# Optimization experiments

Hardware: AMD Instinct MI355X
Metric: run time of the kernel (lower is better)

## Reference

```python
import jax, jax.numpy as jnp
import numpy as np

B, S, D = 2, 2048, 1024
H = 16
HD = D // H  # head_dim = 64


def setup_inputs() -> dict:
    key = jax.random.key(0)
    ks = jax.random.split(key, 6)
    scale = 0.02
    x = jax.random.normal(ks[0], (B, S, D), dtype=jnp.float32)
    Wq = jax.random.normal(ks[1], (D, D), dtype=jnp.float32) * scale
    Wk = jax.random.normal(ks[2], (D, D), dtype=jnp.float32) * scale
    Wv = jax.random.normal(ks[3], (D, D), dtype=jnp.float32) * scale
    Wo = jax.random.normal(ks[4], (D, D), dtype=jnp.float32) * scale
    bo = jax.random.normal(ks[5], (D,), dtype=jnp.float32) * scale
    return {"x": x, "Wq": Wq, "Wk": Wk, "Wv": Wv, "Wo": Wo, "bo": bo}


def reference(x, Wq, Wk, Wv, Wo, bo):
    b, s, d = x.shape
    # QKV projections (no bias, qkv_bias=False)
    Q = (x @ Wq).reshape(b, s, H, HD)
    K = (x @ Wk).reshape(b, s, H, HD)
    V = (x @ Wv).reshape(b, s, H, HD)
    # [b, h, q, k] attention scores
    scores = jnp.einsum('bqhd,bkhd->bhqk', Q, K)
    # causal mask: positions k > q masked to -inf (applied before scaling, as in source;
    # -inf / sqrt(hd) is still -inf so this matches)
    causal = jnp.triu(jnp.ones((s, s), dtype=bool), k=1)
    scores = jnp.where(causal, -jnp.inf, scores)
    att = jax.nn.softmax(scores / jnp.sqrt(jnp.float32(HD)), axis=-1)
    # dropout p=0.0 -> identity
    ctx = jnp.einsum('bhqk,bkhd->bqhd', att, V).reshape(b, s, d)
    return ctx @ Wo + bo
```

## Files before the change

kernel.cpp:

```cpp
#include <hip/hip_runtime.h>

typedef __bf16 bf16;
typedef __attribute__((ext_vector_type(8))) __bf16 bf16x8;
typedef __attribute__((ext_vector_type(4))) __bf16 bf16x4;
typedef __attribute__((ext_vector_type(4))) float floatx4;

#define MFMA16(a, b, c) __builtin_amdgcn_mfma_f32_16x16x32_bf16((a), (b), (c), 0, 0, 0)

static constexpr int BB = 2, SS = 2048, DD = 1024, HH = 16;
static constexpr int MM = BB * SS;
static constexpr int N_QKV = 3 * DD;

__device__ __forceinline__ float exp2c(float x) {
#if __has_builtin(__builtin_amdgcn_exp2f)
    return __builtin_amdgcn_exp2f(x);
#else
    return exp2f(x);
#endif
}

__device__ __forceinline__ void async16(const void* g, void* l) {
    __builtin_amdgcn_global_load_lds(
        (const __attribute__((address_space(1))) unsigned int*)g,
        (__attribute__((address_space(3))) unsigned int*)l, 16, 0, 0);
}

__global__ __launch_bounds__(256) void cvt_x_kernel(const float* __restrict__ x,
                                                    bf16* __restrict__ xb) {
    int i = (blockIdx.x * 256 + threadIdx.x) * 4;
    float4 v = *(const float4*)(x + i);
    bf16x4 o;
    o[0] = (bf16)v.x; o[1] = (bf16)v.y; o[2] = (bf16)v.z; o[3] = (bf16)v.w;
    *(bf16x4*)(xb + i) = o;
}

__global__ __launch_bounds__(256) void cvt_wT_kernel(const float* __restrict__ w0,
                                                     const float* __restrict__ w1,
                                                     const float* __restrict__ w2,
                                                     const float* __restrict__ w3,
                                                     bf16* __restrict__ outT) {
    __shared__ float tile[32][33];
    const float* src = (blockIdx.z == 0) ? w0 : (blockIdx.z == 1) ? w1
                      : (blockIdx.z == 2) ? w2 : w3;
    bf16* dst = outT + (size_t)blockIdx.z * DD * DD;
    int x = blockIdx.x * 32 + threadIdx.x;
    int y0 = blockIdx.y * 32;
    for (int i = threadIdx.y; i < 32; i += 8)
        tile[i][threadIdx.x] = src[(size_t)(y0 + i) * DD + x];
    __syncthreads();
    int xo = y0 + threadIdx.x;
    int yo0 = blockIdx.x * 32;
    for (int i = threadIdx.y; i < 32; i += 8)
        dst[(size_t)(yo0 + i) * DD + xo] = (bf16)tile[threadIdx.x][i];
}

__global__ __launch_bounds__(256) void transpose_v_kernel(const bf16* __restrict__ QKV,
                                                          bf16* __restrict__ Vt_g) {
    __shared__ bf16 t[64][72];
    const int tid = threadIdx.x, srow = tid >> 2, sseg = tid & 3;
    const int bh = blockIdx.y, b = bh >> 4, h = bh & 15;
    const int s0 = blockIdx.x * 64;
    {
        const uint4* p = (const uint4*)(QKV + (size_t)(b * SS + s0 + srow) * N_QKV
                                        + 2 * DD + h * 64 + sseg * 16);
        uint4 a = p[0], c = p[1];
        uint4* d = (uint4*)&t[srow][sseg * 16];
        d[0] = a; d[1] = c;
    }
    __syncthreads();
    bf16x8 o0, o1;
#pragma unroll
    for (int e = 0; e < 8; ++e) o0[e] = t[sseg * 16 + e][srow];
#pragma unroll
    for (int e = 0; e < 8; ++e) o1[e] = t[sseg * 16 + 8 + e][srow];
    uint4* d = (uint4*)(Vt_g + ((size_t)bh * 64 + srow) * SS + s0 + sseg * 16);
    d[0] = *(uint4*)&o0; d[1] = *(uint4*)&o1;
}

template <int BM, int BN, bool OUT_BF16>
__global__ __launch_bounds__(256) void gemm_kernel(const bf16* __restrict__ A,
                                                   const bf16* __restrict__ Bt,
                                                   void* __restrict__ C,
                                                   const float* __restrict__ bias,
                                                   int K, int ldc) {
    constexpr int MT = BM / 32, NT = BN / 32;
    __shared__ bf16 As[BM * 64];
    __shared__ bf16 Bs[BN * 64];
    const int tid = threadIdx.x, wave = tid >> 6, lane = tid & 63;
    const int quad = lane >> 4, l16 = lane & 15;
    const int wm = wave >> 1, wn = wave & 1;
    const int m0 = blockIdx.y * BM, n0 = blockIdx.x * BN;
    const int l8r = lane >> 3, l8c = lane & 7;
    const int gch = ((l8c ^ l8r) * 8);

    floatx4 acc[MT][NT] = {};

    for (int k0 = 0; k0 < K; k0 += 64) {
        __syncthreads();
#pragma unroll
        for (int c = 0; c < BM / 32; ++c) {
            int r = wave * (BM / 4) + c * 8;
            async16(A + (size_t)(m0 + r + l8r) * K + k0 + gch, &As[r * 64]);
        }
#pragma unroll
        for (int c = 0; c < BN / 32; ++c) {
            int r = wave * (BN / 4) + c * 8;
            async16(Bt + (size_t)(n0 + r + l8r) * K + k0 + gch, &Bs[r * 64]);
        }
        __syncthreads();
#pragma unroll
        for (int cc = 0; cc < 2; ++cc) {
            bf16x8 af[MT], bv[NT];
#pragma unroll
            for (int i = 0; i < MT; ++i) {
                int row = wm * (BM / 2) + i * 16 + l16;
                af[i] = *(const bf16x8*)&As[row * 64 + ((cc * 4 + quad) ^ (row & 7)) * 8];
            }
#pragma unroll
            for (int j = 0; j < NT; ++j) {
                int row = wn * (BN / 2) + j * 16 + l16;
                bv[j] = *(const bf16x8*)&Bs[row * 64 + ((cc * 4 + quad) ^ (row & 7)) * 8];
            }
#pragma unroll
            for (int i = 0; i < MT; ++i)
#pragma unroll
                for (int j = 0; j < NT; ++j)
                    acc[i][j] = MFMA16(af[i], bv[j], acc[i][j]);
        }
    }

#pragma unroll
    for (int i = 0; i < MT; ++i)
#pragma unroll
        for (int j = 0; j < NT; ++j)
#pragma unroll
            for (int r = 0; r < 4; ++r) {
                int row = m0 + wm * (BM / 2) + i * 16 + quad * 4 + r;
                int col = n0 + wn * (BN / 2) + j * 16 + l16;
                if (OUT_BF16)
                    ((bf16*)C)[(size_t)row * ldc + col] = (bf16)acc[i][j][r];
                else
                    ((float*)C)[(size_t)row * ldc + col] = acc[i][j][r] + bias[col];
            }
}

__global__ __launch_bounds__(256, 2) void attn_kernel(const bf16* __restrict__ QKV,
                                                      const bf16* __restrict__ Vt_g,
                                                      bf16* __restrict__ ctx) {
    __shared__ __align__(16) bf16 smem[24576];
    bf16* Ks = smem;
    bf16* Vt = smem + 8192;
    bf16* Ps = smem + 16384;
    bf16* Qs = Ps;

    const int tid = threadIdx.x, wave = tid >> 6, lane = tid & 63;
    const int quad = lane >> 4, l16 = lane & 15;
    const int gb = blockIdx.x;
    const int xcd = gb & 7, rr = gb >> 3;
    int bhl, t;
    if (rr < 32) { bhl = rr >> 4;              t = rr & 15; }
    else         { bhl = 2 + ((rr & 31) >> 4); t = 15 - (rr & 15); }
    const int bh = xcd * 4 + bhl;
    const int b = bh >> 4, h = bh & 15;
    const int q0 = t * 128;
    const size_t base = (size_t)(b * SS) * N_QKV;
    const bf16* Vg = Vt_g + (size_t)bh * 64 * SS;
    constexpr float C2 = 0.18033688011112042f;
    const int l8r = lane >> 3, l8c = lane & 7;
    const int gch = (l8c ^ l8r) * 8;
    const int swz = l16 & 7;
    const int nkt = 2 * t + 2;

    {
#pragma unroll
        for (int c = 0; c < 4; ++c) {
            int r0 = wave * 32 + c * 8;
            async16(QKV + base + (size_t)(q0 + r0 + l8r) * N_QKV + h * 64 + gch,
                    Qs + r0 * 64);
        }
#pragma unroll
        for (int c = 0; c < 2; ++c) {
            int r0 = wave * 16 + c * 8;
            async16(QKV + base + (size_t)(r0 + l8r) * N_QKV + DD + h * 64 + gch,
                    Ks + r0 * 64);
            async16(Vg + (size_t)(r0 + l8r) * SS + gch, Vt + r0 * 64);
        }
    }
    __syncthreads();

    bf16x8 qf[2][2];
#pragma unroll
    for (int gg = 0; gg < 2; ++gg)
#pragma unroll
        for (int cc = 0; cc < 2; ++cc) {
            int row = wave * 32 + gg * 16 + l16;
            qf[gg][cc] = *(const bf16x8*)&Qs[row * 64 + ((cc * 4 + quad) ^ swz) * 8];
        }

    bf16x8 onesf = {};
    if (l16 == 0) {
#pragma unroll
        for (int e = 0; e < 8; ++e) onesf[e] = (bf16)1.0f;
    }

    floatx4 accv[2][4] = {};
    floatx4 acc5[2] = {};
    const int qg0 = q0 + wave * 32 + l16;

    for (int kt = 0; kt < nkt; ++kt) {
        const int buf = kt & 1;
        if (kt + 1 < nkt) {
            const int k0n = (kt + 1) * 64;
            const int dst = (buf ^ 1) * 4096;
#pragma unroll
            for (int c = 0; c < 2; ++c) {
                int r0 = wave * 16 + c * 8;
                async16(QKV + base + (size_t)(k0n + r0 + l8r) * N_QKV + DD + h * 64 + gch,
                        Ks + dst + r0 * 64);
                async16(Vg + (size_t)(r0 + l8r) * SS + k0n + gch, Vt + dst + r0 * 64);
            }
        }
        const int k0 = kt * 64;

        floatx4 st[2][4];
#pragma unroll
        for (int j = 0; j < 4; ++j) { st[0][j] = (floatx4){}; st[1][j] = (floatx4){}; }
#pragma unroll
        for (int cc = 0; cc < 2; ++cc)
#pragma unroll
            for (int j = 0; j < 4; ++j) {
                bf16x8 kf = *(const bf16x8*)&Ks[buf * 4096 + (j * 16 + l16) * 64
                                                + ((cc * 4 + quad) ^ swz) * 8];
                st[0][j] = MFMA16(kf, qf[0][cc], st[0][j]);
                st[1][j] = MFMA16(kf, qf[1][cc], st[1][j]);
            }

        if (64 * kt + 63 > q0 + 32 * wave) {
#pragma unroll
            for (int gg = 0; gg < 2; ++gg) {
                const int qq = qg0 + gg * 16;
#pragma unroll
                for (int j = 0; j < 4; ++j) {
                    int kb = k0 + j * 16 + quad * 4;
#pragma unroll
                    for (int r = 0; r < 4; ++r)
                        if (kb + r > qq) st[gg][j][r] = -__builtin_inff();
                }
            }
        }

#pragma unroll
        for (int gg = 0; gg < 2; ++gg)
#pragma unroll
            for (int j = 0; j < 4; ++j) {
                bf16x4 pk4;
#pragma unroll
                for (int r = 0; r < 4; ++r)
                    pk4[r] = (bf16)exp2c(st[gg][j][r] * C2);
                *(bf16x4*)&Ps[wave * 2048 + gg * 1024 + l16 * 64
                              + ((2 * j + (quad >> 1)) ^ swz) * 8 + (quad & 1) * 4] = pk4;
            }

        bf16x8 pf[2][2];
#pragma unroll
        for (int gg = 0; gg < 2; ++gg)
#pragma unroll
            for (int cc = 0; cc < 2; ++cc)
                pf[gg][cc] = *(const bf16x8*)&Ps[wave * 2048 + gg * 1024 + l16 * 64
                                                 + ((cc * 4 + quad) ^ swz) * 8];
#pragma unroll
        for (int cc = 0; cc < 2; ++cc)
#pragma unroll
            for (int j = 0; j < 4; ++j) {
                bf16x8 vt = *(const bf16x8*)&Vt[buf * 4096 + (j * 16 + l16) * 64
                                                + ((cc * 4 + quad) ^ swz) * 8];
                accv[0][j] = MFMA16(pf[0][cc], vt, accv[0][j]);
                accv[1][j] = MFMA16(pf[1][cc], vt, accv[1][j]);
            }
        acc5[0] = MFMA16(pf[0][0], onesf, acc5[0]);
        acc5[0] = MFMA16(pf[0][1], onesf, acc5[0]);
        acc5[1] = MFMA16(pf[1][0], onesf, acc5[1]);
        acc5[1] = MFMA16(pf[1][1], onesf, acc5[1]);

        __syncthreads();
    }

#pragma unroll
    for (int gg = 0; gg < 2; ++gg) {
        float inv[4];
#pragma unroll
        for (int r = 0; r < 4; ++r)
            inv[r] = 1.0f / __shfl(acc5[gg][r], lane & 48, 64);
#pragma unroll
        for (int j = 0; j < 4; ++j)
#pragma unroll
            for (int r = 0; r < 4; ++r) {
                int row = b * SS + q0 + wave * 32 + gg * 16 + quad * 4 + r;
                int col = h * 64 + j * 16 + l16;
                ctx[(size_t)row * DD + col] = (bf16)(accv[gg][j][r] * inv[r]);
            }
    }
}

extern "C" void kernel_launch(void* const* d_in, const int* in_sizes, int n_in,
                              void* d_out, int out_size, void* d_ws, size_t ws_size,
                              hipStream_t stream) {
    const float* x  = (const float*)d_in[0];
    const float* Wq = (const float*)d_in[1];
    const float* Wk = (const float*)d_in[2];
    const float* Wv = (const float*)d_in[3];
    const float* Wo = (const float*)d_in[4];
    const float* bo = (const float*)d_in[5];
    float* out = (float*)d_out;

    char* ws = (char*)d_ws;
    bf16* xb   = (bf16*)ws;
    bf16* WT   = (bf16*)(ws + (size_t)(8  << 20));
    bf16* QKV  = (bf16*)(ws + (size_t)(16 << 20));
    bf16* ctxb = (bf16*)(ws + (size_t)(40 << 20));
    bf16* Vt_g = (bf16*)(ws + (size_t)(48 << 20));

    cvt_x_kernel<<<dim3(MM * DD / (256 * 4)), dim3(256), 0, stream>>>(x, xb);
    cvt_wT_kernel<<<dim3(32, 32, 4), dim3(32, 8), 0, stream>>>(Wq, Wk, Wv, Wo, WT);
    gemm_kernel<128, 128, true><<<dim3(N_QKV / 128, MM / 128), dim3(256), 0, stream>>>(
        xb, WT, QKV, nullptr, DD, N_QKV);
    transpose_v_kernel<<<dim3(SS / 64, BB * HH), dim3(256), 0, stream>>>(QKV, Vt_g);
    attn_kernel<<<dim3(512), dim3(256), 0, stream>>>(QKV, Vt_g, ctxb);
    gemm_kernel<128, 64, false><<<dim3(DD / 64, MM / 128), dim3(256), 0, stream>>>(
        ctxb, WT + (size_t)3 * DD * DD, out, bo, DD, DD);
}
```

Baseline: 173.2 us.

## Merge input conversion kernels and fuse V transpose into QKV GEMM epilogue

Combines the x conversion and the weight transpose-conversion into a single prep kernel, which saves a launch. Removes the separate V transpose kernel. The QKV GEMM blocks that own V columns now write the transposed V layout directly from their accumulators and skip the row-major store. This avoids one extra read and write pass over V and two kernel launches, at the cost of strided 8-byte stores in the GEMM epilogue.

```diff
diff --git a/kernel.cpp b/kernel.cpp
--- a/kernel.cpp
+++ b/kernel.cpp
@@ -25,62 +25,45 @@
         (__attribute__((address_space(3))) unsigned int*)l, 16, 0, 0);
 }
 
-__global__ __launch_bounds__(256) void cvt_x_kernel(const float* __restrict__ x,
-                                                    bf16* __restrict__ xb) {
-    int i = (blockIdx.x * 256 + threadIdx.x) * 4;
-    float4 v = *(const float4*)(x + i);
-    bf16x4 o;
-    o[0] = (bf16)v.x; o[1] = (bf16)v.y; o[2] = (bf16)v.z; o[3] = (bf16)v.w;
-    *(bf16x4*)(xb + i) = o;
-}
-
-__global__ __launch_bounds__(256) void cvt_wT_kernel(const float* __restrict__ w0,
-                                                     const float* __restrict__ w1,
-                                                     const float* __restrict__ w2,
-                                                     const float* __restrict__ w3,
-                                                     bf16* __restrict__ outT) {
-    __shared__ float tile[32][33];
-    const float* src = (blockIdx.z == 0) ? w0 : (blockIdx.z == 1) ? w1
-                      : (blockIdx.z == 2) ? w2 : w3;
-    bf16* dst = outT + (size_t)blockIdx.z * DD * DD;
-    int x = blockIdx.x * 32 + threadIdx.x;
-    int y0 = blockIdx.y * 32;
-    for (int i = threadIdx.y; i < 32; i += 8)
-        tile[i][threadIdx.x] = src[(size_t)(y0 + i) * DD + x];
-    __syncthreads();
-    int xo = y0 + threadIdx.x;
-    int yo0 = blockIdx.x * 32;
-    for (int i = threadIdx.y; i < 32; i += 8)
-        dst[(size_t)(yo0 + i) * DD + xo] = (bf16)tile[threadIdx.x][i];
-}
-
-__global__ __launch_bounds__(256) void transpose_v_kernel(const bf16* __restrict__ QKV,
-                                                          bf16* __restrict__ Vt_g) {
-    __shared__ bf16 t[64][72];
-    const int tid = threadIdx.x, srow = tid >> 2, sseg = tid & 3;
-    const int bh = blockIdx.y, b = bh >> 4, h = bh & 15;
-    const int s0 = blockIdx.x * 64;
-    {
-        const uint4* p = (const uint4*)(QKV + (size_t)(b * SS + s0 + srow) * N_QKV
-                                        + 2 * DD + h * 64 + sseg * 16);
-        uint4 a = p[0], c = p[1];
-        uint4* d = (uint4*)&t[srow][sseg * 16];
-        d[0] = a; d[1] = c;
-    }
-    __syncthreads();
-    bf16x8 o0, o1;
-#pragma unroll
-    for (int e = 0; e < 8; ++e) o0[e] = t[sseg * 16 + e][srow];
-#pragma unroll
-    for (int e = 0; e < 8; ++e) o1[e] = t[sseg * 16 + 8 + e][srow];
-    uint4* d = (uint4*)(Vt_g + ((size_t)bh * 64 + srow) * SS + s0 + sseg * 16);
-    d[0] = *(uint4*)&o0; d[1] = *(uint4*)&o1;
-}
-
-template <int BM, int BN, bool OUT_BF16>
+__global__ __launch_bounds__(256) void prep_kernel(const float* __restrict__ x,
+                                                   bf16* __restrict__ xb,
+                                                   const float* __restrict__ w0,
+                                                   const float* __restrict__ w1,
+                                                   const float* __restrict__ w2,
+                                                   const float* __restrict__ w3,
+                                                   bf16* __restrict__ outT) {
+    const int blk = blockIdx.x, tid = threadIdx.x;
+    if (blk < 4096) {
+        int i = blk * 1024 + tid * 4;
+        float4 v = *(const float4*)(x + i);
+        bf16x4 o;
+        o[0] = (bf16)v.x; o[1] = (bf16)v.y; o[2] = (bf16)v.z; o[3] = (bf16)v.w;
+        *(bf16x4*)(xb + i) = o;
+    } else {
+        __shared__ float tile[32][33];
+        const int wblk = blk - 4096;
+        const int z = wblk >> 10, rem = wblk & 1023;
+        const int by = rem >> 5, bx = rem & 31;
+        const int tx = tid & 31, ty = tid >> 5;
+        const float* src = (z == 0) ? w0 : (z == 1) ? w1 : (z == 2) ? w2 : w3;
+        bf16* dst = outT + (size_t)z * DD * DD;
+        int xc = bx * 32 + tx;
+        int y0 = by * 32;
+        for (int i = ty; i < 32; i += 8)
+            tile[i][tx] = src[(size_t)(y0 + i) * DD + xc];
+        __syncthreads();
+        int xo = y0 + tx;
+        int yo0 = bx * 32;
+        for (int i = ty; i < 32; i += 8)
+            dst[(size_t)(yo0 + i) * DD + xo] = (bf16)tile[tx][i];
+    }
+}
+
+template <int BM, int BN, bool OUT_BF16, bool FUSE_VT>
 __global__ __launch_bounds__(256) void gemm_kernel(const bf16* __restrict__ A,
                                                    const bf16* __restrict__ Bt,
                                                    void* __restrict__ C,
+                                                   bf16* __restrict__ Vt_g,
                                                    const float* __restrict__ bias,
                                                    int K, int ldc) {
     constexpr int MT = BM / 32, NT = BN / 32;
@@ -127,6 +110,24 @@
                 for (int j = 0; j < NT; ++j)
                     acc[i][j] = MFMA16(af[i], bv[j], acc[i][j]);
         }
+    }
+
+    if (FUSE_VT && n0 >= 2048) {
+#pragma unroll
+        for (int i = 0; i < MT; ++i)
+#pragma unroll
+            for (int j = 0; j < NT; ++j) {
+                int grow = m0 + wm * (BM / 2) + i * 16 + quad * 4;
+                int gcol = n0 + wn * (BN / 2) + j * 16 + l16;
+                int bb = grow >> 11, s = grow & (SS - 1);
+                int vcol = gcol - 2048;
+                int hh = vcol >> 6, hd = vcol & 63;
+                bf16x4 pk;
+#pragma unroll
+                for (int r = 0; r < 4; ++r) pk[r] = (bf16)acc[i][j][r];
+                *(bf16x4*)&Vt_g[(((size_t)(bb * 16 + hh)) * 64 + hd) * SS + s] = pk;
+            }
+        return;
     }
 
 #pragma unroll
@@ -320,12 +321,10 @@
     bf16* ctxb = (bf16*)(ws + (size_t)(40 << 20));
     bf16* Vt_g = (bf16*)(ws + (size_t)(48 << 20));
 
-    cvt_x_kernel<<<dim3(MM * DD / (256 * 4)), dim3(256), 0, stream>>>(x, xb);
-    cvt_wT_kernel<<<dim3(32, 32, 4), dim3(32, 8), 0, stream>>>(Wq, Wk, Wv, Wo, WT);
-    gemm_kernel<128, 128, true><<<dim3(N_QKV / 128, MM / 128), dim3(256), 0, stream>>>(
-        xb, WT, QKV, nullptr, DD, N_QKV);
-    transpose_v_kernel<<<dim3(SS / 64, BB * HH), dim3(256), 0, stream>>>(QKV, Vt_g);
+    prep_kernel<<<dim3(8192), dim3(256), 0, stream>>>(x, xb, Wq, Wk, Wv, Wo, WT);
+    gemm_kernel<128, 128, true, true><<<dim3(N_QKV / 128, MM / 128), dim3(256), 0, stream>>>(
+        xb, WT, QKV, Vt_g, nullptr, DD, N_QKV);
     attn_kernel<<<dim3(512), dim3(256), 0, stream>>>(QKV, Vt_g, ctxb);
-    gemm_kernel<128, 64, false><<<dim3(DD / 64, MM / 128), dim3(256), 0, stream>>>(
-        ctxb, WT + (size_t)3 * DD * DD, out, bo, DD, DD);
-}
+    gemm_kernel<128, 64, false, false><<<dim3(DD / 64, MM / 128), dim3(256), 0, stream>>>(
+        ctxb, WT + (size_t)3 * DD * DD, out, nullptr, bo, DD, DD);
+}
```

Result: no change. 173.4 us (+0.1%).
